# Optimization experiments

Hardware: AMD Instinct MI355X
Metric: run time of the kernel (lower is better)

Reference implementation:

```python
import jax, jax.numpy as jnp
import numpy as np


def setup_inputs() -> dict:
    key = jax.random.key(0)
    k1, k2, k3 = jax.random.split(key, 3)
    B, H, S, D = 4, 16, 1024, 64
    return {
        "query": jax.random.normal(k1, (B, H, S, D), dtype=jnp.float32),
        "key": jax.random.normal(k2, (B, H, D, S), dtype=jnp.float32),  # pre-transposed K
        "scale_factor": 8,  # sqrt(head_dim)
        "attention_mask": jnp.zeros((S, S), dtype=jnp.float32),
        "value": jax.random.normal(k3, (B, H, S, D), dtype=jnp.float32),
    }


def reference(query, key, scale_factor, attention_mask, value):
    # Batched equivalent of the per-(b,h) Python loop:
    # scores = Q @ K^T / scale + mask; probs = softmax(scores); out = probs @ V
    scores = jnp.matmul(query, key) / scale_factor  # [B,H,S,S]
    if attention_mask is not None:
        scores = scores + attention_mask  # broadcast [S,S] over [B,H,S,S]
    probs = jax.nn.softmax(scores, axis=-1)
    return jnp.matmul(probs, value)  # [B,H,S,D]
```

## Files before the change

### kernel.cpp

```cpp
#include <hip/hip_runtime.h>

#define BH  64
#define SEQ 1024
#define DIM 64
#define KT  128
#define NT  (SEQ / KT)

typedef __attribute__((ext_vector_type(8))) short  short8;
typedef __attribute__((ext_vector_type(4))) float  floatx4;
typedef __attribute__((ext_vector_type(4))) uint   uintx4;

__device__ __forceinline__ ushort f2bf(float x) {
    union { float f; uint u; } v; v.f = x;
    uint r = v.u + 0x7FFFu + ((v.u >> 16) & 1u);
    return (ushort)(r >> 16);
}
__device__ __forceinline__ uint pack2(float lo, float hi) {
    return (uint)f2bf(lo) | ((uint)f2bf(hi) << 16);
}
__device__ __forceinline__ uint pk2(float lo, float hi) {
    union { float f; uint u; } a, b; a.f = lo; b.f = hi;
    uint au = a.u + 0x8000u, bu = b.u + 0x8000u;
    return __builtin_amdgcn_perm(bu, au, 0x07060302);
}
__device__ __forceinline__ void gld_lds16(const void* g, void* l) {
    __builtin_amdgcn_global_load_lds(
        (const __attribute__((address_space(1))) unsigned int*)g,
        (__attribute__((address_space(3))) unsigned int*)l, 16, 0, 0);
}


__global__ __launch_bounds__(256) void prep_kv_kernel(
    const float* __restrict__ Kin,
    const float* __restrict__ Vin,
    ushort* __restrict__ Kbf, ushort* __restrict__ Vbf)
{
    __shared__ float tile[64][65];
    const int t    = threadIdx.x;
    const int head = blockIdx.y;
    const int s0   = blockIdx.x * 64;
    const int p    = t & 7;

    if (blockIdx.z == 0) {
        const float* ip = Kin + (size_t)head * DIM * SEQ;
#pragma unroll
        for (int i = 0; i < 4; ++i) {
            const int d = (t >> 4) + i * 16;
            const int c = (t & 15) * 4;
            float4 v = *(const float4*)(ip + (size_t)d * SEQ + s0 + c);
            tile[d][c]     = v.x; tile[d][c + 1] = v.y;
            tile[d][c + 2] = v.z; tile[d][c + 3] = v.w;
        }
        __syncthreads();
        char* op = (char*)(Kbf + (size_t)head * SEQ * DIM);
#pragma unroll
        for (int i = 0; i < 2; ++i) {
            const int s  = (t >> 3) + i * 32;
            const int dg = (p ^ (s & 7)) * 8;
            uint4 wv;
            wv.x = pack2(tile[dg + 0][s], tile[dg + 1][s]);
            wv.y = pack2(tile[dg + 2][s], tile[dg + 3][s]);
            wv.z = pack2(tile[dg + 4][s], tile[dg + 5][s]);
            wv.w = pack2(tile[dg + 6][s], tile[dg + 7][s]);
            *(uint4*)(op + (size_t)(s0 + s) * 128 + p * 16) = wv;
        }
    } else {
        const float* ip = Vin + (size_t)head * SEQ * DIM;
#pragma unroll
        for (int i = 0; i < 4; ++i) {
            const int ss = (t >> 4) + i * 16;
            const int c  = (t & 15) * 4;
            float4 v = *(const float4*)(ip + (size_t)(s0 + ss) * DIM + c);
            tile[ss][c]     = v.x; tile[ss][c + 1] = v.y;
            tile[ss][c + 2] = v.z; tile[ss][c + 3] = v.w;
        }
        __syncthreads();
        char* op = (char*)(Vbf + (size_t)head * SEQ * DIM) + (size_t)(s0 >> 6) * 8192;
#pragma unroll
        for (int i = 0; i < 2; ++i) {
            const int d  = (t >> 3) + i * 32;
            const int g  = p ^ (d & 7);
            const int kb = ((g >> 2) * 32) + ((g & 3) * 4);
            uint4 wv;
            wv.x = pack2(tile[kb +  0][d], tile[kb +  1][d]);
            wv.y = pack2(tile[kb +  2][d], tile[kb +  3][d]);
            wv.z = pack2(tile[kb + 16][d], tile[kb + 17][d]);
            wv.w = pack2(tile[kb + 18][d], tile[kb + 19][d]);
            *(uint4*)(op + (size_t)d * 128 + p * 16) = wv;
        }
    }
}

__global__ __launch_bounds__(256) void prep_maskT_kernel(
    const float* __restrict__ m, float* __restrict__ mt)
{
    __shared__ float tile[32][33];
    const int t  = threadIdx.x;
    const int k0 = blockIdx.x * 32;
    const int q0 = blockIdx.y * 32;
    const int tx = t & 31, ty = t >> 5;
#pragma unroll
    for (int i = 0; i < 4; ++i)
        tile[ty + 8 * i][tx] = m[(size_t)(q0 + ty + 8 * i) * SEQ + k0 + tx];
    __syncthreads();
#pragma unroll
    for (int i = 0; i < 4; ++i)
        mt[(size_t)(k0 + ty + 8 * i) * SEQ + q0 + tx] = tile[tx][ty + 8 * i];
}

__global__ __launch_bounds__(512, 4) void mha_mfma2_kernel(
    const float*  __restrict__ Q,
    const ushort* __restrict__ Kbf,
    const int*    __restrict__ scale_p,
    const float*  __restrict__ maskT,
    const ushort* __restrict__ Vbf,
    float*        __restrict__ O)
{
    __shared__ __align__(16) ushort Ks0[KT * 64], Ks1[KT * 64];
    __shared__ __align__(16) ushort Vt0[DIM * KT], Vt1[DIM * KT];

    const int t    = threadIdx.x;
    const int lane = t & 63, w = t >> 6;
    const int li   = lane & 15, quad = lane >> 4;
    const int lx   = li & 7;
    const int bh   = blockIdx.x & 63;
    const int q0   = (blockIdx.x >> 6) * 128;

    const float inv_scale = 1.0f / (float)scale_p[0];

    short8 qa0, qa1;
    {
        const float* Qr = Q + ((size_t)bh * SEQ + q0 + w * 16 + li) * DIM + quad * 8;
        float4 a = *(const float4*)(Qr);
        float4 b = *(const float4*)(Qr + 4);
        float4 c = *(const float4*)(Qr + 32);
        float4 d = *(const float4*)(Qr + 36);
        qa0 = __builtin_bit_cast(short8,
              uintx4{pack2(a.x, a.y), pack2(a.z, a.w), pack2(b.x, b.y), pack2(b.z, b.w)});
        qa1 = __builtin_bit_cast(short8,
              uintx4{pack2(c.x, c.y), pack2(c.z, c.w), pack2(d.x, d.y), pack2(d.z, d.w)});
    }

    floatx4 o[4] = {floatx4{0,0,0,0}, floatx4{0,0,0,0},
                    floatx4{0,0,0,0}, floatx4{0,0,0,0}};
    float l = 0.f;

    const char* KgH = (const char*)(Kbf + (size_t)bh * SEQ * DIM);
    const char* VgH = (const char*)(Vbf + (size_t)bh * SEQ * DIM);
    const int so = w * 2048 + lane * 16;
    char* ksd0 = (char*)Ks0 + w * 2048;
    char* ksd1 = (char*)Ks1 + w * 2048;
    char* vtd0 = (char*)Vt0 + w * 2048;
    char* vtd1 = (char*)Vt1 + w * 2048;

    const float* mrowT = maskT + (size_t)(quad * 4) * SEQ + q0 + w * 16 + li;

    gld_lds16(KgH + so,        ksd0);
    gld_lds16(KgH + so + 1024, ksd0 + 1024);
    gld_lds16(VgH + so,        vtd0);
    gld_lds16(VgH + so + 1024, vtd0 + 1024);
    __builtin_amdgcn_sched_barrier(0);

#pragma unroll 2
    for (int kt = 0; kt < NT; ++kt) {
        const int c = kt & 1;
        const char* ksb = c ? (const char*)Ks1 : (const char*)Ks0;
        const char* vtb = c ? (const char*)Vt1 : (const char*)Vt0;
        char* ksdN = c ? ksd0 : ksd1;
        char* vtdN = c ? vtd0 : vtd1;

        __builtin_amdgcn_s_barrier();

        const int kn = (kt + 1) & (NT - 1);
        {
            const char* kg = KgH + kn * 16384 + so;
            const char* vg = VgH + kn * 16384 + so;
            gld_lds16(kg,        ksdN);
            gld_lds16(kg + 1024, ksdN + 1024);
            gld_lds16(vg,        vtdN);
            gld_lds16(vg + 1024, vtdN + 1024);
        }
        __builtin_amdgcn_sched_barrier(0);
        asm volatile("s_waitcnt vmcnt(4)" ::: "memory");
        __builtin_amdgcn_sched_barrier(0);
        __builtin_amdgcn_s_barrier();

        float mv[32];
#pragma unroll
        for (int n = 0; n < 8; ++n)
#pragma unroll
            for (int r = 0; r < 4; ++r)
                mv[n * 4 + r] = mrowT[(size_t)(kt * KT + n * 16 + r) * SEQ];
        __builtin_amdgcn_sched_barrier(0);

        floatx4 cfr[8];
#pragma unroll
        for (int n = 0; n < 8; ++n) cfr[n] = floatx4{0, 0, 0, 0};
        __builtin_amdgcn_s_setprio(1);
#pragma unroll
        for (int n = 0; n < 8; ++n) {
            const char* krow = ksb + (n * 16 + li) * 128;
            short8 kf0 = *(const short8*)(krow + ((quad ^ lx) * 16));
            short8 kf1 = *(const short8*)(krow + (((4 + quad) ^ lx) * 16));
            cfr[n] = __builtin_amdgcn_mfma_f32_16x16x32_bf16(kf0, qa0, cfr[n], 0, 0, 0);
            cfr[n] = __builtin_amdgcn_mfma_f32_16x16x32_bf16(kf1, qa1, cfr[n], 0, 0, 0);
        }
        __builtin_amdgcn_s_setprio(0);

        uint pw[16];
#pragma unroll
        for (int n = 0; n < 8; ++n) {
            float p0 = __expf(fminf(fmaf(cfr[n][0], inv_scale, mv[n * 4 + 0]), 80.f));
            float p1 = __expf(fminf(fmaf(cfr[n][1], inv_scale, mv[n * 4 + 1]), 80.f));
            float p2 = __expf(fminf(fmaf(cfr[n][2], inv_scale, mv[n * 4 + 2]), 80.f));
            float p3 = __expf(fminf(fmaf(cfr[n][3], inv_scale, mv[n * 4 + 3]), 80.f));
            l += ((p0 + p1) + (p2 + p3));
            pw[n * 2]     = pk2(p0, p1);
            pw[n * 2 + 1] = pk2(p2, p3);
        }
        const short8 pa0 = __builtin_bit_cast(short8, uintx4{pw[0],  pw[1],  pw[2],  pw[3]});
        const short8 pa1 = __builtin_bit_cast(short8, uintx4{pw[4],  pw[5],  pw[6],  pw[7]});
        const short8 pa2 = __builtin_bit_cast(short8, uintx4{pw[8],  pw[9],  pw[10], pw[11]});
        const short8 pa3 = __builtin_bit_cast(short8, uintx4{pw[12], pw[13], pw[14], pw[15]});

        __builtin_amdgcn_s_setprio(1);
#pragma unroll
        for (int n = 0; n < 4; ++n) {
            const char* vrow = vtb + (n * 16 + li) * 128;
            short8 b0 = *(const short8*)(vrow + ((quad ^ lx) * 16));
            short8 b1 = *(const short8*)(vrow + (((4 + quad) ^ lx) * 16));
            o[n] = __builtin_amdgcn_mfma_f32_16x16x32_bf16(pa0, b0, o[n], 0, 0, 0);
            o[n] = __builtin_amdgcn_mfma_f32_16x16x32_bf16(pa1, b1, o[n], 0, 0, 0);
        }
#pragma unroll
        for (int n = 0; n < 4; ++n) {
            const char* vrow = vtb + 8192 + (n * 16 + li) * 128;
            short8 b0 = *(const short8*)(vrow + ((quad ^ lx) * 16));
            short8 b1 = *(const short8*)(vrow + (((4 + quad) ^ lx) * 16));
            o[n] = __builtin_amdgcn_mfma_f32_16x16x32_bf16(pa2, b0, o[n], 0, 0, 0);
            o[n] = __builtin_amdgcn_mfma_f32_16x16x32_bf16(pa3, b1, o[n], 0, 0, 0);
        }
        __builtin_amdgcn_s_setprio(0);
    }

    l += __shfl_xor(l, 16);
    l += __shfl_xor(l, 32);
    float linv[4];
#pragma unroll
    for (int r = 0; r < 4; ++r)
        linv[r] = 1.0f / __shfl(l, quad * 4 + r);

    float* Og = O + ((size_t)bh * SEQ + q0) * DIM;
#pragma unroll
    for (int r = 0; r < 4; ++r) {
#pragma unroll
        for (int n = 0; n < 4; ++n)
            Og[(size_t)(w * 16 + quad * 4 + r) * DIM + n * 16 + li] = o[n][r] * linv[r];
    }
}

extern "C" void kernel_launch(void* const* d_in, const int* in_sizes, int n_in,
                              void* d_out, int out_size, void* d_ws, size_t ws_size,
                              hipStream_t stream) {
    const float* Q     = (const float*)d_in[0];
    const float* K     = (const float*)d_in[1];
    const int*   scale = (const int*)d_in[2];
    const float* mask  = (const float*)d_in[3];
    const float* V     = (const float*)d_in[4];
    float*       Out   = (float*)d_out;

    ushort* Kbf   = (ushort*)d_ws;
    ushort* Vbf   = Kbf + (size_t)BH * SEQ * DIM;
    float*  maskT = (float*)((char*)d_ws + 2 * (size_t)BH * SEQ * DIM * 2);

    prep_kv_kernel<<<dim3(SEQ / 64, BH, 2), 256, 0, stream>>>(K, V, Kbf, Vbf);
    prep_maskT_kernel<<<dim3(SEQ / 32, SEQ / 32), 256, 0, stream>>>(mask, maskT);
    mha_mfma2_kernel<<<dim3(BH * (SEQ / 128)), 512, 0, stream>>>(Q, Kbf, scale, maskT, Vbf, Out);
}
```

Measured before the change: 133.4 us.

## Software-pipeline PV matmul one tile behind QK and softmax

Moves the P·V MFMA block for tile kt-1 to the start of iteration kt, so it overlaps with the next tile's loads and QK work. A zeroed Vt1 buffer with zero P fragments makes the first iteration's deferred PV a no-op, and an epilogue handles the last tile. This aims to hide exp/pack latency behind MFMA work from the prior tile. In exchange it keeps P fragments live across iterations, which raises register pressure, and it adds an LDS zero-fill plus an extra barrier at startup.

After: 134.0 us. No clear change (+0.5%).

```diff
diff --git a/kernel.cpp b/kernel.cpp
--- a/kernel.cpp
+++ b/kernel.cpp
@@ -155,19 +155,50 @@
 
     const float* mrowT = maskT + (size_t)(quad * 4) * SEQ + q0 + w * 16 + li;
 
+    {
+        uint4 z{0, 0, 0, 0};
+        *(uint4*)((char*)Vt1 + t * 32)      = z;
+        *(uint4*)((char*)Vt1 + t * 32 + 16) = z;
+    }
+
     gld_lds16(KgH + so,        ksd0);
     gld_lds16(KgH + so + 1024, ksd0 + 1024);
     gld_lds16(VgH + so,        vtd0);
     gld_lds16(VgH + so + 1024, vtd0 + 1024);
     __builtin_amdgcn_sched_barrier(0);
+    asm volatile("s_waitcnt lgkmcnt(0)" ::: "memory");
+    __builtin_amdgcn_s_barrier();
+
+    short8 paP0 = __builtin_bit_cast(short8, uintx4{0, 0, 0, 0});
+    short8 paP1 = paP0, paP2 = paP0, paP3 = paP0;
 
 #pragma unroll 2
     for (int kt = 0; kt < NT; ++kt) {
         const int c = kt & 1;
-        const char* ksb = c ? (const char*)Ks1 : (const char*)Ks0;
-        const char* vtb = c ? (const char*)Vt1 : (const char*)Vt0;
+        const char* ksb   = c ? (const char*)Ks1 : (const char*)Ks0;
+        const char* vprev = c ? (const char*)Vt0 : (const char*)Vt1;
         char* ksdN = c ? ksd0 : ksd1;
         char* vtdN = c ? vtd0 : vtd1;
+
+        __builtin_amdgcn_s_setprio(1);
+#pragma unroll
+        for (int n = 0; n < 4; ++n) {
+            const char* vrow = vprev + (n * 16 + li) * 128;
+            short8 b0 = *(const short8*)(vrow + ((quad ^ lx) * 16));
+            short8 b1 = *(const short8*)(vrow + (((4 + quad) ^ lx) * 16));
+            o[n] = __builtin_amdgcn_mfma_f32_16x16x32_bf16(paP0, b0, o[n], 0, 0, 0);
+            o[n] = __builtin_amdgcn_mfma_f32_16x16x32_bf16(paP1, b1, o[n], 0, 0, 0);
+        }
+#pragma unroll
+        for (int n = 0; n < 4; ++n) {
+            const char* vrow = vprev + 8192 + (n * 16 + li) * 128;
+            short8 b0 = *(const short8*)(vrow + ((quad ^ lx) * 16));
+            short8 b1 = *(const short8*)(vrow + (((4 + quad) ^ lx) * 16));
+            o[n] = __builtin_amdgcn_mfma_f32_16x16x32_bf16(paP2, b0, o[n], 0, 0, 0);
+            o[n] = __builtin_amdgcn_mfma_f32_16x16x32_bf16(paP3, b1, o[n], 0, 0, 0);
+        }
+        __builtin_amdgcn_s_setprio(0);
+        __builtin_amdgcn_sched_barrier(0);
 
         __builtin_amdgcn_s_barrier();
 
@@ -218,29 +249,30 @@
             pw[n * 2]     = pk2(p0, p1);
             pw[n * 2 + 1] = pk2(p2, p3);
         }
-        const short8 pa0 = __builtin_bit_cast(short8, uintx4{pw[0],  pw[1],  pw[2],  pw[3]});
-        const short8 pa1 = __builtin_bit_cast(short8, uintx4{pw[4],  pw[5],  pw[6],  pw[7]});
-        const short8 pa2 = __builtin_bit_cast(short8, uintx4{pw[8],  pw[9],  pw[10], pw[11]});
-        const short8 pa3 = __builtin_bit_cast(short8, uintx4{pw[12], pw[13], pw[14], pw[15]});
-
-        __builtin_amdgcn_s_setprio(1);
+        paP0 = __builtin_bit_cast(short8, uintx4{pw[0],  pw[1],  pw[2],  pw[3]});
+        paP1 = __builtin_bit_cast(short8, uintx4{pw[4],  pw[5],  pw[6],  pw[7]});
+        paP2 = __builtin_bit_cast(short8, uintx4{pw[8],  pw[9],  pw[10], pw[11]});
+        paP3 = __builtin_bit_cast(short8, uintx4{pw[12], pw[13], pw[14], pw[15]});
+    }
+
+    {
+        const char* vlast = (const char*)Vt1;
 #pragma unroll
         for (int n = 0; n < 4; ++n) {
-            const char* vrow = vtb + (n * 16 + li) * 128;
+            const char* vrow = vlast + (n * 16 + li) * 128;
             short8 b0 = *(const short8*)(vrow + ((quad ^ lx) * 16));
             short8 b1 = *(const short8*)(vrow + (((4 + quad) ^ lx) * 16));
-            o[n] = __builtin_amdgcn_mfma_f32_16x16x32_bf16(pa0, b0, o[n], 0, 0, 0);
-            o[n] = __builtin_amdgcn_mfma_f32_16x16x32_bf16(pa1, b1, o[n], 0, 0, 0);
+            o[n] = __builtin_amdgcn_mfma_f32_16x16x32_bf16(paP0, b0, o[n], 0, 0, 0);
+            o[n] = __builtin_amdgcn_mfma_f32_16x16x32_bf16(paP1, b1, o[n], 0, 0, 0);
         }
 #pragma unroll
         for (int n = 0; n < 4; ++n) {
-            const char* vrow = vtb + 8192 + (n * 16 + li) * 128;
+            const char* vrow = vlast + 8192 + (n * 16 + li) * 128;
             short8 b0 = *(const short8*)(vrow + ((quad ^ lx) * 16));
             short8 b1 = *(const short8*)(vrow + (((4 + quad) ^ lx) * 16));
-            o[n] = __builtin_amdgcn_mfma_f32_16x16x32_bf16(pa2, b0, o[n], 0, 0, 0);
-            o[n] = __builtin_amdgcn_mfma_f32_16x16x32_bf16(pa3, b1, o[n], 0, 0, 0);
-        }
-        __builtin_amdgcn_s_setprio(0);
+            o[n] = __builtin_amdgcn_mfma_f32_16x16x32_bf16(paP2, b0, o[n], 0, 0, 0);
+            o[n] = __builtin_amdgcn_mfma_f32_16x16x32_bf16(paP3, b1, o[n], 0, 0, 0);
+        }
     }
 
     l += __shfl_xor(l, 16);
```
